# Optimization experiments

Hardware: AMD Instinct MI355X
Metric: run time of the kernel (lower is better)

Reference implementation:

```python
import jax, jax.numpy as jnp
import numpy as np

B, S, D, L = 4, 4096, 2048, 4
QH, KVH, WINDOW = 16, 4, 512
HD = D // QH
G = QH // KVH
CAPF = 0.25
EPS = float(jnp.finfo(jnp.float32).eps)  # torch RMSNorm default eps for fp32


def setup_inputs() -> dict:
    key = jax.random.key(0)
    ks = jax.random.split(key, 8)
    s = 0.02
    return {
        "x": jax.random.normal(ks[0], (B, S, D), jnp.float32),
        "router_w": jax.random.normal(ks[1], (1, D), jnp.float32) * s,
        "norm1_w": jnp.ones((L, D), jnp.float32),
        "norm2_w": jnp.ones((L, D), jnp.float32),
        "qkv_w": jax.random.normal(ks[2], (L, (QH + 2 * KVH) * HD, D), jnp.float32) * s,
        "proj_w": jax.random.normal(ks[3], (L, D, D), jnp.float32) * s,
        "fc1_w": jax.random.normal(ks[4], (L, 2 * D, D), jnp.float32) * s,
        "fc2_w": jax.random.normal(ks[5], (L, D, D), jnp.float32) * s,
    }


def rmsnorm(x, w):
    return x * jax.lax.rsqrt(jnp.mean(x * x, -1, keepdims=True) + EPS) * w


def gqa(x, qkv_w, proj_w):
    # x: [B, C, D]; causal sliding-window attention with ALiBi (flash_attn semantics)
    b, c, _ = x.shape
    qkv = x @ qkv_w.T
    q = qkv[..., : QH * HD].reshape(b, c, KVH, G, HD)
    k = qkv[..., QH * HD:(QH + KVH) * HD].reshape(b, c, KVH, HD)
    v = qkv[..., (QH + KVH) * HD:].reshape(b, c, KVH, HD)
    scale = 1.0 / np.sqrt(HD)
    scores = jnp.einsum('bqkgd,bskd->bkgqs', q, k) * scale  # [B,KVH,G,C,C]
    i = jnp.arange(c)[:, None]
    j = jnp.arange(c)[None, :]
    diff = (i - j).astype(jnp.float32)
    mask = (diff >= 0) & (diff <= WINDOW)  # causal + left window
    slopes = jnp.exp2(-((jnp.arange(QH, dtype=jnp.float32) + 1.0) * 8.0 / QH))
    slopes = slopes.reshape(KVH, G, 1, 1)  # q head h = kvh*G + g ordering
    scores = jnp.where(mask, scores - slopes * diff, -jnp.inf)
    p = jax.nn.softmax(scores, axis=-1)
    att = jnp.einsum('bkgqs,bskd->bqkgd', p, v).reshape(b, c, QH * HD)
    return att @ proj_w.T


def swiglu(x, fc1_w, fc2_w):
    h = x @ fc1_w.T
    a, gate = jnp.split(h, 2, axis=-1)
    return (jax.nn.silu(gate) * a) @ fc2_w.T


def reference(x, router_w, norm1_w, norm2_w, qkv_w, proj_w, fc1_w, fc2_w):
    b, s, d = x.shape
    rw = jax.nn.sigmoid(x @ router_w.T)  # [B, S, 1]
    cap = int(s * CAPF)  # training path: capacity = int(seq_len * capacity_factor)
    rws = rw[..., 0]
    _, top_idx = jax.lax.top_k(rws, cap)            # unsorted-by-position top-k
    idx_sorted = jnp.sort(top_idx, axis=1)          # restore sequence order
    order = jnp.argsort(top_idx, axis=1)
    # faithful to source: gathers router_weights at the sort-order permutation
    # indices (values in [0, cap)), exactly as torch.gather(router_weights, 1, router_top_order)
    top_w = jnp.take_along_axis(rws, order, axis=1)[..., None]  # [B, cap, 1]
    lat = jnp.take_along_axis(x, idx_sorted[..., None], axis=1)  # [B, cap, D]
    for l in range(L):
        lat = lat + gqa(rmsnorm(lat, norm1_w[l]), qkv_w[l], proj_w[l])
        lat = lat + swiglu(rmsnorm(lat, norm2_w[l]), fc1_w[l], fc2_w[l])
    lat = lat * top_w
    bidx = jnp.arange(b)[:, None]
    pred = jnp.zeros_like(x).at[bidx, idx_sorted].set(lat)
    decisions = jnp.zeros_like(rw).at[bidx, idx_sorted].set(1.0)
    return pred, rw, decisions
```

## Files before the change

kernel.cpp:

```cpp
#include <hip/hip_runtime.h>
#include <hip/hip_bf16.h>

constexpr int NB = 4;
constexpr int SEQ = 4096;
constexpr int DIM = 2048;
constexpr int NLAYER = 4;
constexpr int NQH = 16;
constexpr int NKVH = 4;
constexpr int WIN = 512;
constexpr int HDIM = 128;
constexpr int CAPN = 1024;
constexpr int MTOK = NB * CAPN;
constexpr int QKVN = (NQH + 2 * NKVH) * HDIM;
constexpr int VOFF = DIM + NKVH * HDIM;
constexpr float EPSF = 1.1920928955078125e-07f;

typedef __hip_bfloat16 bf16;
typedef __bf16 b16x8 __attribute__((ext_vector_type(8)));
typedef __bf16 b16x4 __attribute__((ext_vector_type(4)));
typedef float f32x4 __attribute__((ext_vector_type(4)));

#define MFMA16(a, b, c) __builtin_amdgcn_mfma_f32_16x16x32_bf16((a), (b), (c), 0, 0, 0)

__device__ __forceinline__ void gload_lds16(const void* g, void* l) {
  __builtin_amdgcn_global_load_lds((__attribute__((address_space(1))) void*)(void*)g,
                                   (__attribute__((address_space(3))) void*)l, 16, 0, 0);
}

__global__ __launch_bounds__(256) void cast_kernel(const float* __restrict__ in,
                                                   bf16* __restrict__ out, int n) {
  int i = (blockIdx.x * 256 + threadIdx.x) * 4;
  if (i >= n) return;
  float4 v = *(const float4*)(in + i);
  b16x4 o;
  o[0] = (__bf16)v.x; o[1] = (__bf16)v.y; o[2] = (__bf16)v.z; o[3] = (__bf16)v.w;
  *(b16x4*)((__bf16*)out + i) = o;
}

__global__ __launch_bounds__(256) void cast_fc1_kernel(const float* __restrict__ in,
                                                       bf16* __restrict__ out) {
  int p = blockIdx.x;
  int chunk = p >> 5, w = p & 31;
  int L = (w < 16) ? (chunk * 16 + w) : (DIM + chunk * 16 + (w - 16));
  const float4* spv = (const float4*)(in + (size_t)L * DIM);
  __bf16* op = (__bf16*)out + (size_t)p * DIM;
  int t = threadIdx.x;
#pragma unroll
  for (int j = 0; j < 2; ++j) {
    float4 v = spv[t + j * 256];
    b16x4 o;
    o[0] = (__bf16)v.x; o[1] = (__bf16)v.y; o[2] = (__bf16)v.z; o[3] = (__bf16)v.w;
    *(b16x4*)(op + (t + j * 256) * 4) = o;
  }
}

__global__ __launch_bounds__(256) void router_kernel(const float* __restrict__ x,
                                                     const float* __restrict__ rwt,
                                                     float* __restrict__ rw_out) {
  int tok = blockIdx.x * 4 + (threadIdx.x >> 6);
  int l = threadIdx.x & 63;
  const float* xr = x + (size_t)tok * DIM;
  float s = 0.f;
  for (int c = l; c < DIM; c += 64) s += xr[c] * rwt[c];
  for (int off = 32; off; off >>= 1) s += __shfl_down(s, off);
  if (l == 0) rw_out[tok] = 1.f / (1.f + expf(-s));
}

__global__ __launch_bounds__(256) void rankcnt_kernel(const float* __restrict__ rw,
                                                      int* __restrict__ rank) {
  int blk = blockIdx.x;
  int ic = blk & 15, jc = (blk >> 4) & 15, b = blk >> 8;
  __shared__ float4 svi[64];
  int t = threadIdx.x;
  if (t < 64) svi[t] = ((const float4*)(rw + (size_t)b * SEQ + ic * 256))[t];
  __syncthreads();
  int j = jc * 256 + t;
  float vj = rw[(size_t)b * SEQ + j];
  int r = 0;
#pragma unroll 16
  for (int q = 0; q < 64; ++q) {
    float4 v = svi[q];
    int i = ic * 256 + q * 4;
    r += (v.x > vj || (v.x == vj && (i + 0) < j)) ? 1 : 0;
    r += (v.y > vj || (v.y == vj && (i + 1) < j)) ? 1 : 0;
    r += (v.z > vj || (v.z == vj && (i + 2) < j)) ? 1 : 0;
    r += (v.w > vj || (v.w == vj && (i + 3) < j)) ? 1 : 0;
  }
  atomicAdd(&rank[b * SEQ + j], r);
}

__global__ __launch_bounds__(1024) void select_kernel(const int* __restrict__ rank,
                                                      const float* __restrict__ rw,
                                                      int* __restrict__ idxs,
                                                      float* __restrict__ topw,
                                                      float* __restrict__ dec) {
  int b = blockIdx.x;
  int t = threadIdx.x;
  __shared__ int sr[SEQ];
  __shared__ int scnt[1024];
  for (int i = t; i < SEQ; i += 1024) sr[i] = rank[b * SEQ + i];
  __syncthreads();
  for (int i = t; i < SEQ; i += 1024) dec[(size_t)b * SEQ + i] = (sr[i] < CAPN) ? 1.0f : 0.0f;
  int c = 0;
#pragma unroll
  for (int k = 0; k < 4; ++k) c += (sr[t * 4 + k] < CAPN) ? 1 : 0;
  scnt[t] = c;
  __syncthreads();
  for (int off = 1; off < 1024; off <<= 1) {
    int v = scnt[t];
    int vm = (t >= off) ? scnt[t - off] : 0;
    __syncthreads();
    scnt[t] = v + vm;
    __syncthreads();
  }
  int pos = scnt[t] - c;
  for (int k = 0; k < 4; ++k) {
    int j = t * 4 + k;
    int r = sr[j];
    if (r < CAPN) {
      idxs[b * CAPN + pos] = j;
      topw[b * CAPN + pos] = rw[(size_t)b * SEQ + r];
      pos++;
    }
  }
}

__global__ __launch_bounds__(256) void gather_kernel(const float* __restrict__ x,
                                                     const int* __restrict__ idxs,
                                                     float* __restrict__ lat) {
  int tok = blockIdx.x;
  int b = tok >> 10, i = tok & 1023;
  int src = idxs[b * CAPN + i];
  const float4* spv = (const float4*)(x + ((size_t)b * SEQ + src) * DIM);
  float4* dp = (float4*)(lat + (size_t)tok * DIM);
  int t = threadIdx.x;
  dp[t] = spv[t];
  dp[t + 256] = spv[t + 256];
}

__global__ __launch_bounds__(256) void rmsnorm_kernel(const float* __restrict__ in,
                                                      const float* __restrict__ w,
                                                      bf16* __restrict__ out) {
  int row = blockIdx.x;
  int t = threadIdx.x;
  const float4* spv = (const float4*)(in + (size_t)row * DIM);
  float4 v0 = spv[t], v1 = spv[t + 256];
  float ss = v0.x * v0.x + v0.y * v0.y + v0.z * v0.z + v0.w * v0.w +
             v1.x * v1.x + v1.y * v1.y + v1.z * v1.z + v1.w * v1.w;
  for (int off = 32; off; off >>= 1) ss += __shfl_down(ss, off);
  __shared__ float red[4];
  if ((t & 63) == 0) red[t >> 6] = ss;
  __syncthreads();
  float total = red[0] + red[1] + red[2] + red[3];
  float sc = rsqrtf(total * (1.0f / DIM) + EPSF);
  const float4* wp = (const float4*)w;
  float4 w0 = wp[t], w1 = wp[t + 256];
  __bf16* op = (__bf16*)out + (size_t)row * DIM;
  b16x4 o0, o1;
  o0[0] = (__bf16)(v0.x * w0.x * sc); o0[1] = (__bf16)(v0.y * w0.y * sc);
  o0[2] = (__bf16)(v0.z * w0.z * sc); o0[3] = (__bf16)(v0.w * w0.w * sc);
  o1[0] = (__bf16)(v1.x * w1.x * sc); o1[1] = (__bf16)(v1.y * w1.y * sc);
  o1[2] = (__bf16)(v1.z * w1.z * sc); o1[3] = (__bf16)(v1.w * w1.w * sc);
  *(b16x4*)(op + t * 4) = o0;
  *(b16x4*)(op + 1024 + t * 4) = o1;
}


__device__ __forceinline__ void stage97(const bf16* g, int K, int kt,
                                        bf16* tile, int tid) {
#pragma unroll
  for (int j = 0; j < 4; ++j) {
    int q = j * 4096 + tid * 16;
    int row = q >> 7;
    int sc = ((tid & 7) ^ (row & 7)) << 3;
    gload_lds16((const __bf16*)g + (size_t)row * K + kt * 64 + sc,
                (char*)tile + q);
  }
}

__device__ __forceinline__ b16x8 frag97(const bf16* buf, int row, int ks, int hi) {
  int co = (ks * 32 + hi * 8) ^ ((row & 7) << 3);
  return *(const b16x8*)((const __bf16*)buf + row * 64 + co);
}

template <int MODE>
__global__ __launch_bounds__(256, 3) void gemm97(const bf16* __restrict__ A,
                                                 const bf16* __restrict__ Bw,
                                                 float* __restrict__ Cf,
                                                 bf16* __restrict__ Cb,
                                                 bf16* __restrict__ vTout,
                                                 int N, int K, int nbn) {
  __shared__ __align__(16) bf16 sA[128 * 64];
  __shared__ __align__(16) bf16 sB[128 * 64];
  const int tid = threadIdx.x;
  const int w = tid >> 6, l = tid & 63;
  const int lo = l & 15, hi = l >> 4;
  const int wr = w >> 1, wc = w & 1;
  const int nwg = gridDim.x;
  int bid = blockIdx.x;
  bid = (bid & 7) * (nwg >> 3) + (bid >> 3);
  const int bm = bid / nbn, bn = bid % nbn;
  const bf16* Ab = A + (size_t)bm * 128 * K;
  const bf16* Bb = Bw + (size_t)bn * 128 * K;
  const int nt = K >> 6;

  f32x4 acc[4][4];
#pragma unroll
  for (int i = 0; i < 4; ++i)
#pragma unroll
    for (int j = 0; j < 4; ++j) acc[i][j] = f32x4{0.f, 0.f, 0.f, 0.f};

  for (int t = 0; t < nt; ++t) {
    stage97(Ab, K, t, sA, tid);
    stage97(Bb, K, t, sB, tid);
    __syncthreads();
#pragma unroll
    for (int ks = 0; ks < 2; ++ks) {
      b16x8 af[4], bfm[4];
#pragma unroll
      for (int mi = 0; mi < 4; ++mi)
        af[mi] = frag97(sA, wr * 64 + mi * 16 + lo, ks, hi);
#pragma unroll
      for (int ni = 0; ni < 4; ++ni)
        bfm[ni] = frag97(sB, wc * 64 + ni * 16 + lo, ks, hi);
#pragma unroll
      for (int mi = 0; mi < 4; ++mi)
#pragma unroll
        for (int ni = 0; ni < 4; ++ni)
          acc[mi][ni] = MFMA16(af[mi], bfm[ni], acc[mi][ni]);
    }
    __syncthreads();
  }

#pragma unroll
  for (int mi = 0; mi < 4; ++mi) {
    int row0 = bm * 128 + wr * 64 + mi * 16 + hi * 4;
    if constexpr (MODE == 2) {
#pragma unroll
      for (int j2 = 0; j2 < 2; ++j2) {
        int colL = bn * 64 + wc * 32 + j2 * 16 + lo;
#pragma unroll
        for (int r = 0; r < 4; ++r) {
          float a = acc[mi][2 * j2][r];
          float g = acc[mi][2 * j2 + 1][r];
          float s = g / (1.f + __expf(-g));
          Cb[(size_t)(row0 + r) * DIM + colL] = __float2bfloat16(a * s);
        }
      }
    } else {
#pragma unroll
      for (int ni = 0; ni < 4; ++ni) {
        int col = bn * 128 + wc * 64 + ni * 16 + lo;
#pragma unroll
        for (int r = 0; r < 4; ++r) {
          size_t idx = (size_t)(row0 + r) * N + col;
          float v = acc[mi][ni][r];
          if constexpr (MODE == 3) {
            Cf[idx] += v;
          } else {
            bf16 bv = __float2bfloat16(v);
            Cb[idx] = bv;
            if constexpr (MODE == 1) {
              if (col >= VOFF) {
                int cc = col - VOFF;
                int kvh = cc >> 7, d = cc & 127;
                int row = row0 + r;
                int bb = row >> 10, tk = row & 1023;
                vTout[((size_t)(bb * NKVH + kvh) * HDIM + d) * CAPN + tk] = bv;
              }
            }
          }
        }
      }
    }
  }
}

__global__ __launch_bounds__(256) void attn_kernel(const bf16* __restrict__ qkvb,
                                                   const bf16* __restrict__ vT,
                                                   bf16* __restrict__ attb) {
  const int blk = blockIdx.x;
  const int qc = blk & 31;
  const int kvh = (blk >> 5) & 3;
  const int b = blk >> 7;
  const int w = threadIdx.x >> 6, l = threadIdx.x & 63;
  const int lo = l & 15, hi = l >> 4;
  const int h = kvh * 4 + w;
  const float slope = exp2f(-0.5f * (float)(h + 1));
  const float scale = 0.08838834764831845f;
  __shared__ __align__(16) bf16 p_lds[4][2][16 * 72];
  const __bf16* qp = (const __bf16*)qkvb;
  const __bf16* vtp = (const __bf16*)vT + (size_t)(b * NKVH + kvh) * HDIM * CAPN;
  const size_t tb = (size_t)b * CAPN;
  const int i0b = qc * 32;

  b16x8 aq[2][4];
#pragma unroll
  for (int qt = 0; qt < 2; ++qt) {
    const __bf16* qrow = qp + (tb + i0b + qt * 16 + lo) * QKVN + h * HDIM + hi * 8;
#pragma unroll
    for (int c = 0; c < 4; ++c) aq[qt][c] = *(const b16x8*)(qrow + c * 32);
  }

  f32x4 acc[2][8];
#pragma unroll
  for (int qt = 0; qt < 2; ++qt)
#pragma unroll
    for (int d = 0; d < 8; ++d) acc[qt][d] = f32x4{0.f, 0.f, 0.f, 0.f};
  float mrow[2][4], ssum[2][4];
#pragma unroll
  for (int qt = 0; qt < 2; ++qt)
#pragma unroll
    for (int r = 0; r < 4; ++r) { mrow[qt][r] = -1e30f; ssum[qt][r] = 0.f; }

  const int Ttile = (i0b + 31) & ~63;
  int Btile = i0b - WIN;
  if (Btile < 0) Btile = 0;
  Btile &= ~63;

  for (int j0 = Ttile; j0 >= Btile; j0 -= 64) {
    b16x8 kf[4][4];
#pragma unroll
    for (int jt = 0; jt < 4; ++jt) {
      const __bf16* krow = qp + (tb + j0 + jt * 16 + lo) * QKVN + DIM + kvh * HDIM + hi * 8;
#pragma unroll
      for (int c = 0; c < 4; ++c) kf[jt][c] = *(const b16x8*)(krow + c * 32);
    }
    f32x4 s[2][4];
#pragma unroll
    for (int qt = 0; qt < 2; ++qt)
#pragma unroll
      for (int jt = 0; jt < 4; ++jt) {
        s[qt][jt] = f32x4{0.f, 0.f, 0.f, 0.f};
#pragma unroll
        for (int c = 0; c < 4; ++c) s[qt][jt] = MFMA16(aq[qt][c], kf[jt][c], s[qt][jt]);
      }
    float tmv[2][4];
    int changed = 0;
#pragma unroll
    for (int qt = 0; qt < 2; ++qt) {
#pragma unroll
      for (int r = 0; r < 4; ++r) {
        const int i = i0b + qt * 16 + hi * 4 + r;
        float tm = -1e30f;
#pragma unroll
        for (int jt = 0; jt < 4; ++jt) {
          int d = i - (j0 + jt * 16 + lo);
          float v = (d >= 0 && d <= 512) ? (s[qt][jt][r] * scale - slope * (float)d)
                                         : -1e30f;
          s[qt][jt][r] = v;
          tm = fmaxf(tm, v);
        }
#pragma unroll
        for (int off = 1; off < 16; off <<= 1) tm = fmaxf(tm, __shfl_xor(tm, off));
        tmv[qt][r] = tm;
        changed |= (tm > mrow[qt][r] + 8.0f) ? 1 : 0;
      }
    }
    if (__any(changed)) {
#pragma unroll
      for (int qt = 0; qt < 2; ++qt)
#pragma unroll
        for (int r = 0; r < 4; ++r) {
          float mnew = fmaxf(mrow[qt][r], tmv[qt][r]);
          float corr = (mrow[qt][r] > -1e29f) ? __expf(mrow[qt][r] - mnew) : 0.f;
          ssum[qt][r] *= corr;
#pragma unroll
          for (int d = 0; d < 8; ++d) acc[qt][d][r] *= corr;
          mrow[qt][r] = mnew;
        }
    }
#pragma unroll
    for (int qt = 0; qt < 2; ++qt) {
#pragma unroll
      for (int r = 0; r < 4; ++r) {
        const float m = mrow[qt][r];
        float rs = 0.f;
#pragma unroll
        for (int jt = 0; jt < 4; ++jt) {
          float v = s[qt][jt][r];
          float p = (v > -1e29f) ? __expf(v - m) : 0.f;
          rs += p;
          p_lds[w][qt][(hi * 4 + r) * 72 + jt * 16 + lo] = __float2bfloat16(p);
        }
#pragma unroll
        for (int off = 1; off < 16; off <<= 1) rs += __shfl_xor(rs, off);
        ssum[qt][r] += rs;
      }
    }
#pragma unroll
    for (int ks2 = 0; ks2 < 2; ++ks2) {
      b16x8 pa[2];
      pa[0] = *(const b16x8*)((const __bf16*)p_lds[w][0] + lo * 72 + ks2 * 32 + hi * 8);
      pa[1] = *(const b16x8*)((const __bf16*)p_lds[w][1] + lo * 72 + ks2 * 32 + hi * 8);
#pragma unroll
      for (int dh = 0; dh < 2; ++dh) {
        b16x8 bv[4];
#pragma unroll
        for (int dd = 0; dd < 4; ++dd) {
          int d = dh * 4 + dd;
          bv[dd] = *(const b16x8*)(vtp + (size_t)(d * 16 + lo) * CAPN + j0 + ks2 * 32 + hi * 8);
        }
#pragma unroll
        for (int qt = 0; qt < 2; ++qt)
#pragma unroll
          for (int dd = 0; dd < 4; ++dd)
            acc[qt][dh * 4 + dd] = MFMA16(pa[qt], bv[dd], acc[qt][dh * 4 + dd]);
      }
    }
  }
#pragma unroll
  for (int qt = 0; qt < 2; ++qt)
#pragma unroll
    for (int d = 0; d < 8; ++d)
#pragma unroll
      for (int r = 0; r < 4; ++r) {
        int row = i0b + qt * 16 + hi * 4 + r;
        attb[(tb + row) * DIM + h * HDIM + d * 16 + lo] =
            __float2bfloat16(acc[qt][d][r] / ssum[qt][r]);
      }
}

__global__ __launch_bounds__(256) void scatter_kernel(const float* __restrict__ lat,
                                                      const int* __restrict__ idxs,
                                                      const float* __restrict__ topw,
                                                      float* __restrict__ pred) {
  int tok = blockIdx.x;
  int b = tok >> 10, i = tok & 1023;
  int dst = idxs[b * CAPN + i];
  float wv = topw[b * CAPN + i];
  const float4* spv = (const float4*)(lat + (size_t)tok * DIM);
  float4* dp = (float4*)(pred + ((size_t)b * SEQ + dst) * DIM);
  int t = threadIdx.x;
  float4 v = spv[t];
  v.x *= wv; v.y *= wv; v.z *= wv; v.w *= wv;
  dp[t] = v;
  v = spv[t + 256];
  v.x *= wv; v.y *= wv; v.z *= wv; v.w *= wv;
  dp[t + 256] = v;
}

extern "C" void kernel_launch(void* const* d_in, const int* in_sizes, int n_in,
                              void* d_out, int out_size, void* d_ws, size_t ws_size,
                              hipStream_t stream) {
  const float* x        = (const float*)d_in[0];
  const float* router_w = (const float*)d_in[1];
  const float* norm1_w  = (const float*)d_in[2];
  const float* norm2_w  = (const float*)d_in[3];
  const float* qkv_w    = (const float*)d_in[4];
  const float* proj_w   = (const float*)d_in[5];
  const float* fc1_w    = (const float*)d_in[6];
  const float* fc2_w    = (const float*)d_in[7];

  float* pred   = (float*)d_out;
  float* rw_out = pred + (size_t)NB * SEQ * DIM;
  float* dec    = rw_out + (size_t)NB * SEQ;

  char* ws = (char*)d_ws;
  float* lat  = (float*)ws; ws += (size_t)MTOK * DIM * 4;
  bf16* xn    = (bf16*)ws;  ws += (size_t)MTOK * DIM * 2;
  bf16* qkvb  = (bf16*)ws;  ws += (size_t)MTOK * QKVN * 2;
  bf16* attb  = (bf16*)ws;  ws += (size_t)MTOK * DIM * 2;
  int* rank   = (int*)ws;   ws += (size_t)NB * SEQ * 4;
  int* idxs   = (int*)ws;   ws += (size_t)NB * CAPN * 4;
  float* topw = (float*)ws; ws += (size_t)NB * CAPN * 4;

  char* sp = (char*)pred;
  sp += (size_t)MTOK * (2 * DIM) * 2;
  bf16* wq = (bf16*)sp; sp += (size_t)QKVN * DIM * 2;
  bf16* wp = (bf16*)sp; sp += (size_t)DIM * DIM * 2;
  bf16* w1 = (bf16*)sp; sp += (size_t)(2 * DIM) * DIM * 2;
  bf16* w2 = (bf16*)sp; sp += (size_t)DIM * DIM * 2;
  bf16* vT = (bf16*)sp; sp += (size_t)NB * NKVH * HDIM * CAPN * 2;

  router_kernel<<<NB * SEQ / 4, 256, 0, stream>>>(x, router_w, rw_out);
  hipMemsetAsync(rank, 0, (size_t)NB * SEQ * 4, stream);
  rankcnt_kernel<<<NB * 256, 256, 0, stream>>>(rw_out, rank);
  select_kernel<<<NB, 1024, 0, stream>>>(rank, rw_out, idxs, topw, dec);
  gather_kernel<<<MTOK, 256, 0, stream>>>(x, idxs, lat);

  for (int l = 0; l < NLAYER; ++l) {
    cast_kernel<<<(QKVN * DIM) / 1024, 256, 0, stream>>>(qkv_w + (size_t)l * QKVN * DIM, wq, QKVN * DIM);
    cast_kernel<<<(DIM * DIM) / 1024, 256, 0, stream>>>(proj_w + (size_t)l * DIM * DIM, wp, DIM * DIM);
    cast_fc1_kernel<<<2 * DIM, 256, 0, stream>>>(fc1_w + (size_t)l * 2 * DIM * DIM, w1);
    cast_kernel<<<(DIM * DIM) / 1024, 256, 0, stream>>>(fc2_w + (size_t)l * DIM * DIM, w2, DIM * DIM);

    rmsnorm_kernel<<<MTOK, 256, 0, stream>>>(lat, norm1_w + (size_t)l * DIM, xn);
    gemm97<1><<<(MTOK / 128) * (QKVN / 128), 256, 0, stream>>>(
        xn, wq, nullptr, qkvb, vT, QKVN, DIM, QKVN / 128);
    attn_kernel<<<NB * NKVH * 32, 256, 0, stream>>>(qkvb, vT, attb);
    gemm97<3><<<(MTOK / 128) * (DIM / 128), 256, 0, stream>>>(
        attb, wp, lat, nullptr, nullptr, DIM, DIM, DIM / 128);

    rmsnorm_kernel<<<MTOK, 256, 0, stream>>>(lat, norm2_w + (size_t)l * DIM, xn);
    gemm97<2><<<(MTOK / 128) * (2 * DIM / 128), 256, 0, stream>>>(
        xn, w1, nullptr, attb, nullptr, 2 * DIM, DIM, 2 * DIM / 128);
    gemm97<3><<<(MTOK / 128) * (DIM / 128), 256, 0, stream>>>(
        attb, w2, lat, nullptr, nullptr, DIM, DIM, DIM / 128);
  }

  hipMemsetAsync(pred, 0, (size_t)NB * SEQ * DIM * 4, stream);
  scatter_kernel<<<MTOK, 256, 0, stream>>>(lat, idxs, topw, pred);
}
```

Baseline: 1.498 ms.

## Double-buffer K tiles in LDS with async loads in attention kernel

```diff
diff --git a/kernel.cpp b/kernel.cpp
--- a/kernel.cpp
+++ b/kernel.cpp
@@ -288,6 +288,7 @@
   const int h = kvh * 4 + w;
   const float slope = exp2f(-0.5f * (float)(h + 1));
   const float scale = 0.08838834764831845f;
+  __shared__ __align__(16) bf16 sK[2][64 * 128];
   __shared__ __align__(16) bf16 p_lds[4][2][16 * 72];
   const __bf16* qp = (const __bf16*)qkvb;
   const __bf16* vtp = (const __bf16*)vT + (size_t)(b * NKVH + kvh) * HDIM * CAPN;
@@ -318,23 +319,49 @@
   if (Btile < 0) Btile = 0;
   Btile &= ~63;
 
+  auto stageK = [&](int j0, int bufi) {
+    const __bf16* gb = qp + (tb + j0) * QKVN + DIM + kvh * HDIM;
+#pragma unroll
+    for (int jj = 0; jj < 4; ++jj) {
+      int q = jj * 4096 + threadIdx.x * 16;
+      int rowd = q >> 8;
+      int ch = (q >> 4) & 15;
+      int chs = ch ^ (rowd & 7);
+      gload_lds16(gb + (size_t)rowd * QKVN + chs * 8, (char*)sK[bufi] + q);
+    }
+  };
+
+  stageK(Ttile, 0);
+  asm volatile("s_waitcnt vmcnt(0)" ::: "memory");
+  __builtin_amdgcn_sched_barrier(0);
+  __syncthreads();
+
+  int cur = 0;
   for (int j0 = Ttile; j0 >= Btile; j0 -= 64) {
-    b16x8 kf[4][4];
-#pragma unroll
-    for (int jt = 0; jt < 4; ++jt) {
-      const __bf16* krow = qp + (tb + j0 + jt * 16 + lo) * QKVN + DIM + kvh * HDIM + hi * 8;
-#pragma unroll
-      for (int c = 0; c < 4; ++c) kf[jt][c] = *(const b16x8*)(krow + c * 32);
-    }
+    const bool more = (j0 - 64) >= Btile;
+    if (more) stageK(j0 - 64, cur ^ 1);
+    const __bf16* kb = (const __bf16*)sK[cur];
     f32x4 s[2][4];
 #pragma unroll
-    for (int qt = 0; qt < 2; ++qt)
-#pragma unroll
-      for (int jt = 0; jt < 4; ++jt) {
-        s[qt][jt] = f32x4{0.f, 0.f, 0.f, 0.f};
-#pragma unroll
-        for (int c = 0; c < 4; ++c) s[qt][jt] = MFMA16(aq[qt][c], kf[jt][c], s[qt][jt]);
-      }
+    for (int jtp = 0; jtp < 2; ++jtp) {
+      b16x8 kf[2][4];
+#pragma unroll
+      for (int jt2 = 0; jt2 < 2; ++jt2) {
+        int rr = (jtp * 2 + jt2) * 16 + lo;
+#pragma unroll
+        for (int c = 0; c < 4; ++c)
+          kf[jt2][c] = *(const b16x8*)(kb + rr * 128 + (((c * 4 + hi) ^ (rr & 7)) << 3));
+      }
+#pragma unroll
+      for (int qt = 0; qt < 2; ++qt)
+#pragma unroll
+        for (int jt2 = 0; jt2 < 2; ++jt2) {
+          f32x4 sv = f32x4{0.f, 0.f, 0.f, 0.f};
+#pragma unroll
+          for (int c = 0; c < 4; ++c) sv = MFMA16(aq[qt][c], kf[jt2][c], sv);
+          s[qt][jtp * 2 + jt2] = sv;
+        }
+    }
     float tmv[2][4];
     int changed = 0;
 #pragma unroll
@@ -407,6 +434,12 @@
           for (int dd = 0; dd < 4; ++dd)
             acc[qt][dh * 4 + dd] = MFMA16(pa[qt], bv[dd], acc[qt][dh * 4 + dd]);
       }
+    }
+    if (more) {
+      asm volatile("s_waitcnt vmcnt(0)" ::: "memory");
+      __builtin_amdgcn_sched_barrier(0);
+      __syncthreads();
+      cur ^= 1;
     }
   }
 #pragma unroll
```

Result: slower. 1.563 ms (+4.4%).

## Compute softmax row sums via MFMA with ones and defer row-max reduction

Applied to the files above, without the earlier changes.

```diff
diff --git a/kernel.cpp b/kernel.cpp
--- a/kernel.cpp
+++ b/kernel.cpp
@@ -302,16 +302,23 @@
     for (int c = 0; c < 4; ++c) aq[qt][c] = *(const b16x8*)(qrow + c * 32);
   }
 
+  b16x8 ONES;
+#pragma unroll
+  for (int j = 0; j < 8; ++j) ONES[j] = (__bf16)1.0f;
+
   f32x4 acc[2][8];
+  f32x4 accs[2];
+#pragma unroll
+  for (int qt = 0; qt < 2; ++qt) {
+#pragma unroll
+    for (int d = 0; d < 8; ++d) acc[qt][d] = f32x4{0.f, 0.f, 0.f, 0.f};
+    accs[qt] = f32x4{0.f, 0.f, 0.f, 0.f};
+  }
+  float mrow[2][4];
 #pragma unroll
   for (int qt = 0; qt < 2; ++qt)
 #pragma unroll
-    for (int d = 0; d < 8; ++d) acc[qt][d] = f32x4{0.f, 0.f, 0.f, 0.f};
-  float mrow[2][4], ssum[2][4];
-#pragma unroll
-  for (int qt = 0; qt < 2; ++qt)
-#pragma unroll
-    for (int r = 0; r < 4; ++r) { mrow[qt][r] = -1e30f; ssum[qt][r] = 0.f; }
+    for (int r = 0; r < 4; ++r) mrow[qt][r] = -1e30f;
 
   const int Ttile = (i0b + 31) & ~63;
   int Btile = i0b - WIN;
@@ -319,52 +326,57 @@
   Btile &= ~63;
 
   for (int j0 = Ttile; j0 >= Btile; j0 -= 64) {
-    b16x8 kf[4][4];
-#pragma unroll
-    for (int jt = 0; jt < 4; ++jt) {
-      const __bf16* krow = qp + (tb + j0 + jt * 16 + lo) * QKVN + DIM + kvh * HDIM + hi * 8;
-#pragma unroll
-      for (int c = 0; c < 4; ++c) kf[jt][c] = *(const b16x8*)(krow + c * 32);
-    }
     f32x4 s[2][4];
 #pragma unroll
-    for (int qt = 0; qt < 2; ++qt)
-#pragma unroll
-      for (int jt = 0; jt < 4; ++jt) {
-        s[qt][jt] = f32x4{0.f, 0.f, 0.f, 0.f};
-#pragma unroll
-        for (int c = 0; c < 4; ++c) s[qt][jt] = MFMA16(aq[qt][c], kf[jt][c], s[qt][jt]);
-      }
-    float tmv[2][4];
-    int changed = 0;
+    for (int jtp = 0; jtp < 2; ++jtp) {
+      b16x8 kf[2][4];
+#pragma unroll
+      for (int jt2 = 0; jt2 < 2; ++jt2) {
+        const __bf16* krow =
+            qp + (tb + j0 + (jtp * 2 + jt2) * 16 + lo) * QKVN + DIM + kvh * HDIM + hi * 8;
+#pragma unroll
+        for (int c = 0; c < 4; ++c) kf[jt2][c] = *(const b16x8*)(krow + c * 32);
+      }
+#pragma unroll
+      for (int qt = 0; qt < 2; ++qt)
+#pragma unroll
+        for (int jt2 = 0; jt2 < 2; ++jt2) {
+          f32x4 sv = f32x4{0.f, 0.f, 0.f, 0.f};
+#pragma unroll
+          for (int c = 0; c < 4; ++c) sv = MFMA16(aq[qt][c], kf[jt2][c], sv);
+          s[qt][jtp * 2 + jt2] = sv;
+        }
+    }
+    int flag = 0;
 #pragma unroll
     for (int qt = 0; qt < 2; ++qt) {
 #pragma unroll
       for (int r = 0; r < 4; ++r) {
         const int i = i0b + qt * 16 + hi * 4 + r;
-        float tm = -1e30f;
+        const float thr = mrow[qt][r] + 8.0f;
 #pragma unroll
         for (int jt = 0; jt < 4; ++jt) {
           int d = i - (j0 + jt * 16 + lo);
           float v = (d >= 0 && d <= 512) ? (s[qt][jt][r] * scale - slope * (float)d)
                                          : -1e30f;
           s[qt][jt][r] = v;
-          tm = fmaxf(tm, v);
-        }
-#pragma unroll
-        for (int off = 1; off < 16; off <<= 1) tm = fmaxf(tm, __shfl_xor(tm, off));
-        tmv[qt][r] = tm;
-        changed |= (tm > mrow[qt][r] + 8.0f) ? 1 : 0;
-      }
-    }
-    if (__any(changed)) {
+          flag |= (v > thr) ? 1 : 0;
+        }
+      }
+    }
+    if (__any(flag)) {
 #pragma unroll
       for (int qt = 0; qt < 2; ++qt)
 #pragma unroll
         for (int r = 0; r < 4; ++r) {
-          float mnew = fmaxf(mrow[qt][r], tmv[qt][r]);
+          float tm = -1e30f;
+#pragma unroll
+          for (int jt = 0; jt < 4; ++jt) tm = fmaxf(tm, s[qt][jt][r]);
+#pragma unroll
+          for (int off = 1; off < 16; off <<= 1) tm = fmaxf(tm, __shfl_xor(tm, off));
+          float mnew = fmaxf(mrow[qt][r], tm);
           float corr = (mrow[qt][r] > -1e29f) ? __expf(mrow[qt][r] - mnew) : 0.f;
-          ssum[qt][r] *= corr;
+          accs[qt][r] *= corr;
 #pragma unroll
           for (int d = 0; d < 8; ++d) acc[qt][d][r] *= corr;
           mrow[qt][r] = mnew;
@@ -375,17 +387,12 @@
 #pragma unroll
       for (int r = 0; r < 4; ++r) {
         const float m = mrow[qt][r];
-        float rs = 0.f;
 #pragma unroll
         for (int jt = 0; jt < 4; ++jt) {
           float v = s[qt][jt][r];
           float p = (v > -1e29f) ? __expf(v - m) : 0.f;
-          rs += p;
           p_lds[w][qt][(hi * 4 + r) * 72 + jt * 16 + lo] = __float2bfloat16(p);
         }
-#pragma unroll
-        for (int off = 1; off < 16; off <<= 1) rs += __shfl_xor(rs, off);
-        ssum[qt][r] += rs;
       }
     }
 #pragma unroll
@@ -394,6 +401,8 @@
       pa[0] = *(const b16x8*)((const __bf16*)p_lds[w][0] + lo * 72 + ks2 * 32 + hi * 8);
       pa[1] = *(const b16x8*)((const __bf16*)p_lds[w][1] + lo * 72 + ks2 * 32 + hi * 8);
 #pragma unroll
+      for (int qt = 0; qt < 2; ++qt) accs[qt] = MFMA16(pa[qt], ONES, accs[qt]);
+#pragma unroll
       for (int dh = 0; dh < 2; ++dh) {
         b16x8 bv[4];
 #pragma unroll
@@ -417,7 +426,7 @@
       for (int r = 0; r < 4; ++r) {
         int row = i0b + qt * 16 + hi * 4 + r;
         attb[(tb + row) * DIM + h * HDIM + d * 16 + lo] =
-            __float2bfloat16(acc[qt][d][r] / ssum[qt][r]);
+            __float2bfloat16(acc[qt][d][r] / accs[qt][r]);
       }
 }
 
```

New measurement: 1.500 ms. No clear change (+0.1%).
